# Kernel optimization log

Hardware: AMD Instinct MI355X
Metric: run time of the kernel (lower is better)

## Reference

```python
import jax, jax.numpy as jnp
import numpy as np
import math

EPS = 1e-8
DIM, HEADS, K = 256, 8, 16
HD = DIM // HEADS
B, N, PDIM = 4, 4096, 3


def _layernorm(x, w, b, eps=1e-5):
    m = jnp.mean(x, axis=-1, keepdims=True)
    v = jnp.mean((x - m) ** 2, axis=-1, keepdims=True)
    return (x - m) * jax.lax.rsqrt(v + eps) * w + b


def setup_inputs() -> dict:
    key = jax.random.key(0)
    ks = jax.random.split(key, 16)
    s = 0.02
    d = {
        'x': jax.random.normal(ks[0], (B, N, DIM), jnp.float32),
        'positions': jax.random.uniform(ks[1], (B, N, PDIM), jnp.float32) * 0.5,  # inside unit ball
        'c': jnp.ones((1,), jnp.float32),
        'time_emb': jax.random.normal(ks[2], (B, DIM), jnp.float32),
        'Wq': jax.random.normal(ks[3], (DIM, DIM), jnp.float32) * s,
        'bq': jnp.zeros((DIM,), jnp.float32),
        'Wk': jax.random.normal(ks[4], (DIM, DIM), jnp.float32) * s,
        'bk': jnp.zeros((DIM,), jnp.float32),
        'Wv': jax.random.normal(ks[5], (DIM, DIM), jnp.float32) * s,
        'bv': jnp.zeros((DIM,), jnp.float32),
        'Wo': jax.random.normal(ks[6], (DIM, DIM), jnp.float32) * s,
        'bo': jnp.zeros((DIM,), jnp.float32),
        'W1': jax.random.normal(ks[7], (DIM, 4 * DIM), jnp.float32) * s,
        'b1': jnp.zeros((4 * DIM,), jnp.float32),
        'W2': jax.random.normal(ks[8], (4 * DIM, DIM), jnp.float32) * s,
        'b2': jnp.zeros((DIM,), jnp.float32),
        'ln1_w': jnp.ones((DIM,), jnp.float32),
        'ln1_b': jnp.zeros((DIM,), jnp.float32),
        'ln2_w': jnp.ones((DIM,), jnp.float32),
        'ln2_b': jnp.zeros((DIM,), jnp.float32),
        'log_tau': jnp.zeros((), jnp.float32),
    }
    return d


def _poincare_dist_matrix(pos, c):
    # pos: [B,N,P], c: scalar > 0. Returns [B,N,N] with d[b,i,j] = dist(pos[b,j], pos[b,i])
    sq = jnp.sum(pos ** 2, axis=-1)                      # [B,N]
    diff2 = (sq[:, :, None] + sq[:, None, :]
             - 2.0 * jnp.einsum('bip,bjp->bij', pos, pos))
    diff2 = jnp.maximum(diff2, 0.0)
    num = 2.0 * c * diff2
    den = (1.0 - c * sq[:, :, None]) * (1.0 - c * sq[:, None, :])
    arg = jnp.maximum(1.0 + num / (den + EPS), 1.0)
    return jnp.arccosh(arg) / jnp.sqrt(c)


def reference(x, positions, c, time_emb, Wq, bq, Wk, bk, Wv, bv, Wo, bo,
              W1, b1, W2, b2, ln1_w, ln1_b, ln2_w, ln2_b, log_tau):
    c_s = jnp.squeeze(c)
    x_res = x
    h = _layernorm(x, ln1_w, ln1_b) + time_emb[:, None, :]

    q = (h @ Wq + bq).reshape(B, N, HEADS, HD).transpose(0, 2, 1, 3)  # [B,H,N,hd]
    k = (h @ Wk + bk).reshape(B, N, HEADS, HD).transpose(0, 2, 1, 3)
    v = (h @ Wv + bv).reshape(B, N, HEADS, HD).transpose(0, 2, 1, 3)

    # pairwise hyperbolic distances + kNN (no_grad in original)
    dist = jax.lax.stop_gradient(_poincare_dist_matrix(positions, c_s))  # [B,N,N]
    neg_vals, idx = jax.lax.top_k(-dist, K)          # smallest-K distances
    attn_dists = -neg_vals                            # [B,N,K]

    # gather neighbor keys/values: out[b,h,n,j,d] = k[b,h,idx[b,n,j],d]
    idx_flat = idx.reshape(B, 1, N * K, 1)            # broadcast over heads, hd
    k_g = jnp.take_along_axis(k, idx_flat, axis=2).reshape(B, HEADS, N, K, HD)
    v_g = jnp.take_along_axis(v, idx_flat, axis=2).reshape(B, HEADS, N, K, HD)

    feat = jnp.einsum('bhnd,bhnkd->bhnk', q, k_g) / math.sqrt(HD)
    tau = jnp.exp(log_tau) + EPS
    scores = feat - attn_dists[:, None, :, :] / tau
    probs = jax.nn.softmax(scores, axis=-1)
    attn = jnp.einsum('bhnk,bhnkd->bhnd', probs, v_g)
    attn = attn.transpose(0, 2, 1, 3).reshape(B, N, DIM)

    x2 = x_res + attn @ Wo + bo
    ff = jax.nn.gelu(_layernorm(x2, ln2_w, ln2_b) @ W1 + b1, approximate=False) @ W2 + b2
    return x2 + ff
```

## Files before the change

### kernel.cpp

```cpp
#include <hip/hip_runtime.h>
#include <math.h>

namespace {

constexpr int kBatch = 4;
constexpr int kN = 4096;
constexpr int kDim = 256;
constexpr int kHeads = 8;
constexpr int kK = 16;
constexpr float kEps = 1e-8f;

using u16 = unsigned short;
typedef __attribute__((ext_vector_type(8))) short short8;
typedef __attribute__((ext_vector_type(8))) u16 u16x8;
typedef __attribute__((ext_vector_type(4))) float f32x4;

__device__ __forceinline__ float b2f(u16 u) {
  union { unsigned int i; float f; } x; x.i = ((unsigned int)u) << 16; return x.f;
}
__device__ __forceinline__ u16 f2b(float f) {
  union { float f; unsigned int i; } x; x.f = f;
  unsigned int r = x.i + 0x7fffu + ((x.i >> 16) & 1u);
  return (u16)(r >> 16);
}
__device__ __forceinline__ float gelu_exact(float x) {
  return 0.5f * x * (1.0f + erff(x * 0.70710678118654752f));
}
__device__ __forceinline__ void load_lds16(const u16* g, u16* l) {
  __builtin_amdgcn_global_load_lds(
      (const __attribute__((address_space(1))) unsigned int*)g,
      (__attribute__((address_space(3))) unsigned int*)l, 16, 0, 0);
}

template<bool ADD_TEMB>
__device__ __forceinline__ void ln_body(
    const float* __restrict__ x, const float* __restrict__ w,
    const float* __restrict__ bb, const float* __restrict__ temb,
    u16* __restrict__ out, int gt) {
  int row = gt >> 6;
  int lane = gt & 63;
  const float4* xr = (const float4*)(x + (size_t)row * kDim);
  float4 v = xr[lane];
  float s = v.x + v.y + v.z + v.w;
  #pragma unroll
  for (int off = 32; off; off >>= 1) s += __shfl_xor(s, off);
  float mean = s * (1.0f / kDim);
  float dx = v.x - mean, dy = v.y - mean, dz = v.z - mean, dw = v.w - mean;
  float ss = dx * dx + dy * dy + dz * dz + dw * dw;
  #pragma unroll
  for (int off = 32; off; off >>= 1) ss += __shfl_xor(ss, off);
  float rstd = rsqrtf(ss * (1.0f / kDim) + 1e-5f);
  float4 wv = ((const float4*)w)[lane];
  float4 bv = ((const float4*)bb)[lane];
  float ox = dx * rstd * wv.x + bv.x;
  float oy = dy * rstd * wv.y + bv.y;
  float oz = dz * rstd * wv.z + bv.z;
  float ow = dw * rstd * wv.w + bv.w;
  if (ADD_TEMB) {
    int bi = row >> 12;
    float4 t = ((const float4*)(temb + (size_t)bi * kDim))[lane];
    ox += t.x; oy += t.y; oz += t.z; ow += t.w;
  }
  ushort4 ob;
  ob.x = f2b(ox); ob.y = f2b(oy); ob.z = f2b(oz); ob.w = f2b(ow);
  ((ushort4*)(out + (size_t)row * kDim))[lane] = ob;
}

__global__ __launch_bounds__(1024, 2) void front_kernel(
    const float* __restrict__ pos, const float* __restrict__ cptr,
    int* __restrict__ idx_out, float* __restrict__ dist_out,
    const float* __restrict__ x, const float* __restrict__ ln1w,
    const float* __restrict__ ln1b, const float* __restrict__ temb,
    u16* __restrict__ h_out,
    const float* __restrict__ Wq, const float* __restrict__ Wk,
    const float* __restrict__ Wv, const float* __restrict__ Wo,
    const float* __restrict__ W1, const float* __restrict__ W2,
    u16* __restrict__ Tq, u16* __restrict__ Tk,
    u16* __restrict__ Tv, u16* __restrict__ To,
    u16* __restrict__ T1, u16* __restrict__ T2) {
  __shared__ float4 ps[kN];
  int tid = threadIdx.x;
  int bx = blockIdx.x;

  if (bx >= 1024) {
    if (bx < 1216) {
      int sub = tid >> 8, stid = tid & 255;
      int task = (bx - 1024) * 4 + sub;
      float* tt = (float*)ps + sub * 1056;
      int seg = task >> 8, e = task & 255;
      const float* W; u16* T; int Kin, Nin, kt, nt;
      if (seg == 0) {
        int which = e >> 6, tl = e & 63;
        W = which == 0 ? Wq : which == 1 ? Wk : which == 2 ? Wv : Wo;
        T = which == 0 ? Tq : which == 1 ? Tk : which == 2 ? Tv : To;
        Kin = 256; Nin = 256; kt = tl >> 3; nt = tl & 7;
      } else if (seg == 1) {
        W = W1; T = T1; Kin = 256; Nin = 1024; kt = e >> 5; nt = e & 31;
      } else {
        W = W2; T = T2; Kin = 1024; Nin = 256; kt = e >> 3; nt = e & 7;
      }
      int tx = stid & 31, ty = stid >> 5;
      #pragma unroll
      for (int rr = 0; rr < 4; ++rr) {
        int r = rr * 8 + ty;
        tt[r * 33 + tx] = W[(size_t)(kt * 32 + r) * Nin + nt * 32 + tx];
      }
      __syncthreads();
      #pragma unroll
      for (int rr = 0; rr < 4; ++rr) {
        int r = rr * 8 + ty;
        T[(size_t)(nt * 32 + r) * Kin + kt * 32 + tx] = f2b(tt[tx * 33 + r]);
      }
    } else {
      ln_body<true>(x, ln1w, ln1b, temb, h_out, (bx - 1216) * 1024 + tid);
    }
    return;
  }

  int wave = tid >> 6, ln = tid & 63;
  int row = bx * 16 + wave;
  int b = row >> 12;
  float c = cptr[0];
  const float* pb = pos + (size_t)b * kN * 3;
  for (int j = tid; j < kN; j += 1024) {
    float px = pb[j * 3 + 0], py = pb[j * 3 + 1], pz = pb[j * 3 + 2];
    ps[j] = make_float4(px, py, pz, c * (px * px + py * py + pz * pz));
  }
  __syncthreads();

  int i = row & (kN - 1);
  float4 pi = ps[i];
  float wi = pi.w, oi = 1.0f - wi;
  float sx = 2.0f * c * pi.x, sy = 2.0f * c * pi.y, sz = 2.0f * c * pi.z;

  auto numden = [&](int j, float& num, float& den) {
    float4 pj = ps[j];
    float tt = wi + pj.w;
    tt = fmaf(-sx, pj.x, tt);
    tt = fmaf(-sy, pj.y, tt);
    tt = fmaf(-sz, pj.z, tt);
    num = fmaxf(tt, 0.0f);
    den = fmaf(-oi, pj.w, oi);
  };
  auto packkey = [&](float num, float den, int j) -> unsigned {
    float r = num * __builtin_amdgcn_rcpf(den);
    union { float f; unsigned u; } cv; cv.f = r;
    return (cv.u & 0xFFFFF000u) | (unsigned)j;
  };
  auto inflate = [&](unsigned T) -> float {
    union { unsigned u; float f; } tv; tv.u = T & 0xFFFFF000u;
    return fmaf(tv.f, 0.001f, tv.f);
  };

  float n0, d0;
  numden(ln, n0, d0);
  unsigned lpk = packkey(n0, d0, ln);
  #pragma unroll
  for (int kk = 2; kk <= 64; kk <<= 1) {
    #pragma unroll
    for (int jj = kk >> 1; jj >= 1; jj >>= 1) {
      unsigned ov = (unsigned)__shfl_xor((int)lpk, jj);
      bool keepMin = (((ln & kk) == 0) == ((ln & jj) == 0));
      bool less = ov < lpk;
      if (keepMin ? less : !less) lpk = ov;
    }
  }
  float Tf = inflate((unsigned)__builtin_amdgcn_readlane((int)lpk, 15));

  auto processGroup = [&](float num, float den, int base) {
    unsigned long long m = __ballot(num < Tf * den);
    if (m) {
      unsigned cpk = packkey(num, den, base + ln);
      do {
        int src = __ffsll(m) - 1;
        m &= m - 1;
        unsigned npk = (unsigned)__builtin_amdgcn_readlane((int)cpk, src);
        unsigned pv = (unsigned)__builtin_amdgcn_update_dpp(
            0, (int)lpk, 0x111 , 0xF, 0xF, false);
        bool gt = lpk > npk;
        bool take = gt && ((ln == 0) || (pv <= npk));
        lpk = take ? npk : (gt ? pv : lpk);
      } while (m);
      Tf = inflate((unsigned)__builtin_amdgcn_readlane((int)lpk, 15));
    }
  };

  int t = 1;
  for (; t + 3 < 64; t += 4) {
    float a0, b0, a1, b1, a2, b2, a3, b3;
    numden(ln + (t + 0) * 64, a0, b0);
    numden(ln + (t + 1) * 64, a1, b1);
    numden(ln + (t + 2) * 64, a2, b2);
    numden(ln + (t + 3) * 64, a3, b3);
    processGroup(a0, b0, (t + 0) * 64);
    processGroup(a1, b1, (t + 1) * 64);
    processGroup(a2, b2, (t + 2) * 64);
    processGroup(a3, b3, (t + 3) * 64);
  }
  for (; t < 64; ++t) {
    float a0, b0;
    numden(ln + t * 64, a0, b0);
    processGroup(a0, b0, t * 64);
  }

  if (ln < kK) {
    int j = (int)(lpk & 0xFFFu);
    float4 pj = ps[j];
    float tt = wi + pj.w;
    tt = fmaf(-sx, pj.x, tt);
    tt = fmaf(-sy, pj.y, tt);
    tt = fmaf(-sz, pj.z, tt);
    float num = 2.0f * fmaxf(tt, 0.0f);
    float den = fmaf(-oi, pj.w, oi) + kEps;
    float arg = fmaxf(1.0f + num / den, 1.0f);
    float rs = 1.0f / sqrtf(c);
    idx_out[(size_t)row * kK + ln] = j;
    dist_out[(size_t)row * kK + ln] = acoshf(arg) * rs;
  }
}

template<int EPI, int BN>
__device__ __forceinline__ void gemm_body(
    const u16* __restrict__ A, const u16* __restrict__ Bt,
    const float* __restrict__ bias, const float* __restrict__ R,
    float* __restrict__ Cf, u16* __restrict__ Cbf,
    int N, int K, int bx, int by) {
  constexpr int NI = BN / 32;
  constexpr int BK = 64;
  __shared__ u16 Al[128 * BK];
  __shared__ u16 Bl[BN * BK];
  int tid = threadIdx.x;
  int wv = tid >> 6, ln = tid & 63;
  int wr = wv >> 1, wc = wv & 1;
  int lhi = ln >> 4, llo = ln & 15;
  int bm = bx * 128, bn = by * BN;

  f32x4 zero = {0.f, 0.f, 0.f, 0.f};
  f32x4 acc[4][NI];
  #pragma unroll
  for (int mi = 0; mi < 4; ++mi)
    #pragma unroll
    for (int ni = 0; ni < NI; ++ni) acc[mi][ni] = zero;

  for (int k0 = 0; k0 < K; k0 += BK) {
    if (k0) __syncthreads();
    #pragma unroll
    for (int i = 0; i < 128 * BK / (8 * 256); ++i) {
      int f = i * 256 + tid;
      int r = f >> 3, o = f & 7;
      load_lds16(A + (size_t)(bm + r) * K + k0 + ((o ^ (r & 7)) << 3),
                 &Al[(i * 256 + wv * 64) * 8]);
    }
    #pragma unroll
    for (int i = 0; i < BN * BK / (8 * 256); ++i) {
      int f = i * 256 + tid;
      int r = f >> 3, o = f & 7;
      load_lds16(Bt + (size_t)(bn + r) * K + k0 + ((o ^ (r & 7)) << 3),
                 &Bl[(i * 256 + wv * 64) * 8]);
    }
    __syncthreads();
    #pragma unroll
    for (int ks = 0; ks < BK; ks += 32) {
      short8 af[4], bf[NI];
      #pragma unroll
      for (int mi = 0; mi < 4; ++mi) {
        int row = wr * 64 + mi * 16 + llo;
        int oct = ((ks >> 3) + lhi) ^ (llo & 7);
        af[mi] = *(const short8*)&Al[row * BK + oct * 8];
      }
      #pragma unroll
      for (int ni = 0; ni < NI; ++ni) {
        int row = wc * (BN / 2) + ni * 16 + llo;
        int oct = ((ks >> 3) + lhi) ^ (llo & 7);
        bf[ni] = *(const short8*)&Bl[row * BK + oct * 8];
      }
      #pragma unroll
      for (int mi = 0; mi < 4; ++mi)
        #pragma unroll
        for (int ni = 0; ni < NI; ++ni)
          acc[mi][ni] = __builtin_amdgcn_mfma_f32_16x16x32_bf16(
              af[mi], bf[ni], acc[mi][ni], 0, 0, 0);
    }
  }

  #pragma unroll
  for (int mi = 0; mi < 4; ++mi) {
    #pragma unroll
    for (int r = 0; r < 4; ++r) {
      int row = bm + wr * 64 + mi * 16 + lhi * 4 + r;
      #pragma unroll
      for (int ni = 0; ni < NI; ++ni) {
        int col = bn + wc * (BN / 2) + ni * 16 + llo;
        float val = acc[mi][ni][r] + bias[col];
        if (EPI == 1) {
          val += R[(size_t)row * N + col];
          Cf[(size_t)row * N + col] = val;
        } else {
          if (EPI == 2) val = gelu_exact(val);
          Cbf[(size_t)row * N + col] = f2b(val);
        }
      }
    }
  }
}

template<int EPI, int BN, int NY>
__global__ __launch_bounds__(256) void gemm_swz_kernel(
    const u16* __restrict__ A, const u16* __restrict__ Bt,
    const float* __restrict__ bias, const float* __restrict__ R,
    float* __restrict__ Cf, u16* __restrict__ Cbf, int N, int K) {
  int cpx = gridDim.x >> 3;
  int orig = blockIdx.x;
  int swz = (orig & 7) * cpx + (orig >> 3);
  int bx = swz / NY, by = swz % NY;
  gemm_body<EPI, BN>(A, Bt, bias, R, Cf, Cbf, N, K, bx, by);
}

__global__ __launch_bounds__(256) void qkv_kernel(
    const u16* __restrict__ A,
    const u16* __restrict__ Bq, const u16* __restrict__ Bk, const u16* __restrict__ Bv,
    const float* __restrict__ bq, const float* __restrict__ bk, const float* __restrict__ bv,
    u16* __restrict__ q, u16* __restrict__ k, u16* __restrict__ v) {
  int cpx = gridDim.x >> 3;
  int orig = blockIdx.x;
  int swz = (orig & 7) * cpx + (orig >> 3);
  int bx = swz / 6, y = swz % 6;
  int sel = y >> 1;
  const u16* Bt = sel == 0 ? Bq : sel == 1 ? Bk : Bv;
  const float* bias = sel == 0 ? bq : sel == 1 ? bk : bv;
  u16* C = sel == 0 ? q : sel == 1 ? k : v;
  gemm_body<0, 128>(A, Bt, bias, nullptr, nullptr, C, 256, 256, bx, y & 1);
}

__global__ __launch_bounds__(512) void wo_ln_kernel(
    const u16* __restrict__ A, const u16* __restrict__ Bt,
    const float* __restrict__ bo, const float* __restrict__ xres,
    const float* __restrict__ ln2w, const float* __restrict__ ln2b,
    float* __restrict__ x2, u16* __restrict__ tln) {
  __shared__ u16 Al[64 * 64];
  __shared__ u16 Bl[256 * 64];
  __shared__ float red[4][64][2];
  int tid = threadIdx.x;
  int wv = tid >> 6, ln = tid & 63;
  int wr = wv >> 2, wc = wv & 3;
  int lhi = ln >> 4, llo = ln & 15;
  int bm = blockIdx.x * 64;

  f32x4 zero = {0.f, 0.f, 0.f, 0.f};
  f32x4 acc[2][4];
  #pragma unroll
  for (int mi = 0; mi < 2; ++mi)
    #pragma unroll
    for (int ni = 0; ni < 4; ++ni) acc[mi][ni] = zero;

  for (int k0 = 0; k0 < 256; k0 += 64) {
    if (k0) __syncthreads();
    {
      int f = tid, r = f >> 3, o = f & 7;
      load_lds16(A + (size_t)(bm + r) * 256 + k0 + ((o ^ (r & 7)) << 3),
                 &Al[(wv * 64) * 8]);
    }
    #pragma unroll
    for (int i = 0; i < 4; ++i) {
      int f = i * 512 + tid, r = f >> 3, o = f & 7;
      load_lds16(Bt + (size_t)r * 256 + k0 + ((o ^ (r & 7)) << 3),
                 &Bl[((i * 8 + wv) * 64) * 8]);
    }
    __syncthreads();
    #pragma unroll
    for (int ks = 0; ks < 64; ks += 32) {
      short8 af[2], bf[4];
      #pragma unroll
      for (int mi = 0; mi < 2; ++mi) {
        int row = wr * 32 + mi * 16 + llo;
        int oct = ((ks >> 3) + lhi) ^ (llo & 7);
        af[mi] = *(const short8*)&Al[row * 64 + oct * 8];
      }
      #pragma unroll
      for (int ni = 0; ni < 4; ++ni) {
        int brow = wc * 64 + ni * 16 + llo;
        int oct = ((ks >> 3) + lhi) ^ (llo & 7);
        bf[ni] = *(const short8*)&Bl[brow * 64 + oct * 8];
      }
      #pragma unroll
      for (int mi = 0; mi < 2; ++mi)
        #pragma unroll
        for (int ni = 0; ni < 4; ++ni)
          acc[mi][ni] = __builtin_amdgcn_mfma_f32_16x16x32_bf16(
              af[mi], bf[ni], acc[mi][ni], 0, 0, 0);
    }
  }

  float psum[2][4], psq[2][4];
  #pragma unroll
  for (int mi = 0; mi < 2; ++mi) {
    #pragma unroll
    for (int r = 0; r < 4; ++r) {
      int row = bm + wr * 32 + mi * 16 + lhi * 4 + r;
      float s = 0.0f, q = 0.0f;
      #pragma unroll
      for (int ni = 0; ni < 4; ++ni) {
        int col = wc * 64 + ni * 16 + llo;
        float v = acc[mi][ni][r] + bo[col] + xres[(size_t)row * 256 + col];
        acc[mi][ni][r] = v;
        s += v;
        q = fmaf(v, v, q);
      }
      #pragma unroll
      for (int off = 1; off < 16; off <<= 1) {
        s += __shfl_xor(s, off);
        q += __shfl_xor(q, off);
      }
      psum[mi][r] = s; psq[mi][r] = q;
    }
  }
  if (llo == 0) {
    #pragma unroll
    for (int mi = 0; mi < 2; ++mi)
      #pragma unroll
      for (int r = 0; r < 4; ++r) {
        int rl = wr * 32 + mi * 16 + lhi * 4 + r;
        red[wc][rl][0] = psum[mi][r];
        red[wc][rl][1] = psq[mi][r];
      }
  }
  __syncthreads();
  constexpr float rn = 1.0f / 256.0f;
  #pragma unroll
  for (int mi = 0; mi < 2; ++mi) {
    #pragma unroll
    for (int r = 0; r < 4; ++r) {
      int rl = wr * 32 + mi * 16 + lhi * 4 + r;
      int row = bm + rl;
      float S = red[0][rl][0] + red[1][rl][0] + red[2][rl][0] + red[3][rl][0];
      float Q = red[0][rl][1] + red[1][rl][1] + red[2][rl][1] + red[3][rl][1];
      float mean = S * rn;
      float var = Q * rn - mean * mean;
      float rstd = rsqrtf(var + 1e-5f);
      #pragma unroll
      for (int ni = 0; ni < 4; ++ni) {
        int col = wc * 64 + ni * 16 + llo;
        float v = acc[mi][ni][r];
        x2[(size_t)row * 256 + col] = v;
        tln[(size_t)row * 256 + col] =
            f2b((v - mean) * rstd * ln2w[col] + ln2b[col]);
      }
    }
  }
}

__global__ __launch_bounds__(256) void attn_kernel(
    const u16* __restrict__ q, const u16* __restrict__ k,
    const u16* __restrict__ v, const int* __restrict__ nidx,
    const float* __restrict__ ndist, const float* __restrict__ log_tau,
    u16* __restrict__ out) {
  int t = blockIdx.x * 256 + threadIdx.x;
  int h = t & (kHeads - 1);
  int row = t >> 3;
  int b = row >> 12;
  float rtau = 1.0f / (expf(log_tau[0]) + kEps);
  const u16x8* qr = (const u16x8*)(q + (size_t)row * kDim + h * 32);
  float qf[32];
  #pragma unroll
  for (int cch = 0; cch < 4; ++cch) {
    u16x8 u = qr[cch];
    #pragma unroll
    for (int e = 0; e < 8; ++e) qf[cch * 8 + e] = b2f(u[e]);
  }

  int njs[kK];
  float sc[kK];
  const int* ir = nidx + (size_t)row * kK;
  const float* dr = ndist + (size_t)row * kK;
  float smax = -1e30f;
  #pragma unroll
  for (int j = 0; j < kK; ++j) {
    int nj = ir[j];
    njs[j] = nj;
    const u16x8* kr = (const u16x8*)(k + ((size_t)b * kN + nj) * kDim + h * 32);
    float dot = 0.0f;
    #pragma unroll
    for (int cch = 0; cch < 4; ++cch) {
      u16x8 u = kr[cch];
      #pragma unroll
      for (int e = 0; e < 8; ++e) dot = fmaf(qf[cch * 8 + e], b2f(u[e]), dot);
    }
    float s = dot * 0.17677669529663687f - dr[j] * rtau;
    sc[j] = s;
    smax = fmaxf(smax, s);
  }
  float sum = 0.0f;
  #pragma unroll
  for (int j = 0; j < kK; ++j) { sc[j] = expf(sc[j] - smax); sum += sc[j]; }
  float rsum = 1.0f / sum;
  float o[32];
  #pragma unroll
  for (int d = 0; d < 32; ++d) o[d] = 0.0f;
  #pragma unroll
  for (int j = 0; j < kK; ++j) {
    float p = sc[j] * rsum;
    const u16x8* vr = (const u16x8*)(v + ((size_t)b * kN + njs[j]) * kDim + h * 32);
    #pragma unroll
    for (int cch = 0; cch < 4; ++cch) {
      u16x8 u = vr[cch];
      #pragma unroll
      for (int e = 0; e < 8; ++e) o[cch * 8 + e] = fmaf(p, b2f(u[e]), o[cch * 8 + e]);
    }
  }
  u16x8* orow = (u16x8*)(out + (size_t)row * kDim + h * 32);
  #pragma unroll
  for (int cch = 0; cch < 4; ++cch) {
    u16x8 po;
    #pragma unroll
    for (int e = 0; e < 8; ++e) po[e] = f2b(o[cch * 8 + e]);
    orow[cch] = po;
  }
}

}

extern "C" void kernel_launch(void* const* d_in, const int* in_sizes, int n_in,
                              void* d_out, int out_size, void* d_ws, size_t ws_size,
                              hipStream_t stream) {
  const float* x    = (const float*)d_in[0];
  const float* pos  = (const float*)d_in[1];
  const float* c    = (const float*)d_in[2];
  const float* temb = (const float*)d_in[3];
  const float* Wq   = (const float*)d_in[4];
  const float* bq   = (const float*)d_in[5];
  const float* Wk   = (const float*)d_in[6];
  const float* bk   = (const float*)d_in[7];
  const float* Wv   = (const float*)d_in[8];
  const float* bv   = (const float*)d_in[9];
  const float* Wo   = (const float*)d_in[10];
  const float* bo   = (const float*)d_in[11];
  const float* W1   = (const float*)d_in[12];
  const float* b1   = (const float*)d_in[13];
  const float* W2   = (const float*)d_in[14];
  const float* b2   = (const float*)d_in[15];
  const float* ln1w = (const float*)d_in[16];
  const float* ln1b = (const float*)d_in[17];
  const float* ln2w = (const float*)d_in[18];
  const float* ln2b = (const float*)d_in[19];
  const float* ltau = (const float*)d_in[20];

  const size_t MB = 1ull << 20;
  char* w = (char*)d_ws;
  u16*   h_bf  = (u16*)(w + 0 * MB);
  u16*   qb    = (u16*)(w + 8 * MB);
  u16*   kb    = (u16*)(w + 16 * MB);
  u16*   vb    = (u16*)(w + 24 * MB);
  u16*   attnb = (u16*)(w + 32 * MB);
  float* x2    = (float*)(w + 40 * MB);
  u16*   g_bf  = (u16*)(w + 56 * MB);
  u16*   wq_t  = (u16*)(w + 88 * MB);
  u16*   wk_t  = wq_t + 65536;
  u16*   wv_t  = wq_t + 2 * 65536;
  u16*   wo_t  = wq_t + 3 * 65536;
  u16*   w1_t  = (u16*)(w + 89 * MB);
  u16*   w2_t  = (u16*)(w + 89 * MB + 512 * 1024);
  int*   kidx  = (int*)(w + 90 * MB);
  float* kdst  = (float*)(w + 91 * MB);
  u16*   tln   = h_bf;

  hipLaunchKernelGGL(front_kernel, dim3(2240), dim3(1024), 0, stream,
                     pos, c, kidx, kdst,
                     x, ln1w, ln1b, temb, h_bf,
                     Wq, Wk, Wv, Wo, W1, W2, wq_t, wk_t, wv_t, wo_t, w1_t, w2_t);
  hipLaunchKernelGGL(qkv_kernel, dim3(768), dim3(256), 0, stream,
                     h_bf, wq_t, wk_t, wv_t, bq, bk, bv, qb, kb, vb);
  hipLaunchKernelGGL(attn_kernel, dim3(512), dim3(256), 0, stream,
                     qb, kb, vb, kidx, kdst, ltau, attnb);
  hipLaunchKernelGGL(wo_ln_kernel, dim3(256), dim3(512), 0, stream,
                     attnb, wo_t, bo, x, ln2w, ln2b, x2, tln);
  hipLaunchKernelGGL((gemm_swz_kernel<2, 128, 8>), dim3(1024), dim3(256), 0, stream,
                     tln, w1_t, b1, nullptr, (float*)nullptr, g_bf, 1024, 256);
  hipLaunchKernelGGL((gemm_swz_kernel<1, 64, 4>), dim3(512), dim3(256), 0, stream,
                     g_bf, w2_t, b2, x2, (float*)d_out, (u16*)nullptr, 256, 1024);
}
```

Measured before the change: 163.2 us.

## Fuse kNN attention into Wo projection + LayerNorm kernel via LDS tile

The separate attention kernel is folded into the Wo GEMM + LayerNorm kernel. Each 512-thread block first computes attention for its 64 rows × 8 heads and writes the bf16 result straight into a swizzled 64x256 LDS A-tile, then runs the Wo GEMM from LDS. This removes one launch and the global write/read round trip of the attention output. In exchange, LDS per block grows and the attention phase now runs with only 256 blocks of 512 threads, which lowers parallelism for the gather-heavy part and may reduce occupancy.

New measurement: 161.6 us. No clear change (-1.0%).

```diff
diff --git a/kernel.cpp b/kernel.cpp
--- a/kernel.cpp
+++ b/kernel.cpp
@@ -332,19 +332,86 @@
   gemm_body<0, 128>(A, Bt, bias, nullptr, nullptr, C, 256, 256, bx, y & 1);
 }
 
-__global__ __launch_bounds__(512) void wo_ln_kernel(
-    const u16* __restrict__ A, const u16* __restrict__ Bt,
-    const float* __restrict__ bo, const float* __restrict__ xres,
+__global__ __launch_bounds__(512) void awo_ln_kernel(
+    const u16* __restrict__ q, const u16* __restrict__ k,
+    const u16* __restrict__ v, const int* __restrict__ nidx,
+    const float* __restrict__ ndist, const float* __restrict__ log_tau,
+    const u16* __restrict__ Bt, const float* __restrict__ bo,
+    const float* __restrict__ xres,
     const float* __restrict__ ln2w, const float* __restrict__ ln2b,
     float* __restrict__ x2, u16* __restrict__ tln) {
-  __shared__ u16 Al[64 * 64];
+  __shared__ u16 Al[64 * 256];
   __shared__ u16 Bl[256 * 64];
   __shared__ float red[4][64][2];
   int tid = threadIdx.x;
+  int bm = blockIdx.x * 64;
+
+  {
+    int rl = tid >> 3, h = tid & 7;
+    int row = bm + rl;
+    int b = row >> 12;
+    float rtau = 1.0f / (expf(log_tau[0]) + kEps);
+    const u16x8* qr = (const u16x8*)(q + (size_t)row * kDim + h * 32);
+    float qf[32];
+    #pragma unroll
+    for (int cch = 0; cch < 4; ++cch) {
+      u16x8 u = qr[cch];
+      #pragma unroll
+      for (int e = 0; e < 8; ++e) qf[cch * 8 + e] = b2f(u[e]);
+    }
+    int njs[kK];
+    float sc[kK];
+    const int* ir = nidx + (size_t)row * kK;
+    const float* dr = ndist + (size_t)row * kK;
+    float smax = -1e30f;
+    #pragma unroll
+    for (int j = 0; j < kK; ++j) {
+      int nj = ir[j];
+      njs[j] = nj;
+      const u16x8* kr = (const u16x8*)(k + ((size_t)b * kN + nj) * kDim + h * 32);
+      float dot = 0.0f;
+      #pragma unroll
+      for (int cch = 0; cch < 4; ++cch) {
+        u16x8 u = kr[cch];
+        #pragma unroll
+        for (int e = 0; e < 8; ++e) dot = fmaf(qf[cch * 8 + e], b2f(u[e]), dot);
+      }
+      float s = dot * 0.17677669529663687f - dr[j] * rtau;
+      sc[j] = s;
+      smax = fmaxf(smax, s);
+    }
+    float sum = 0.0f;
+    #pragma unroll
+    for (int j = 0; j < kK; ++j) { sc[j] = expf(sc[j] - smax); sum += sc[j]; }
+    float rsum = 1.0f / sum;
+    float o[32];
+    #pragma unroll
+    for (int d = 0; d < 32; ++d) o[d] = 0.0f;
+    #pragma unroll
+    for (int j = 0; j < kK; ++j) {
+      float p = sc[j] * rsum;
+      const u16x8* vr = (const u16x8*)(v + ((size_t)b * kN + njs[j]) * kDim + h * 32);
+      #pragma unroll
+      for (int cch = 0; cch < 4; ++cch) {
+        u16x8 u = vr[cch];
+        #pragma unroll
+        for (int e = 0; e < 8; ++e) o[cch * 8 + e] = fmaf(p, b2f(u[e]), o[cch * 8 + e]);
+      }
+    }
+    #pragma unroll
+    for (int cch = 0; cch < 4; ++cch) {
+      u16x8 po;
+      #pragma unroll
+      for (int e = 0; e < 8; ++e) po[e] = f2b(o[cch * 8 + e]);
+      int oct = h * 4 + cch;
+      *(u16x8*)&Al[rl * 256 + ((oct ^ (rl & 7)) << 3)] = po;
+    }
+  }
+  __syncthreads();
+
   int wv = tid >> 6, ln = tid & 63;
   int wr = wv >> 2, wc = wv & 3;
   int lhi = ln >> 4, llo = ln & 15;
-  int bm = blockIdx.x * 64;
 
   f32x4 zero = {0.f, 0.f, 0.f, 0.f};
   f32x4 acc[2][4];
@@ -355,11 +422,6 @@
 
   for (int k0 = 0; k0 < 256; k0 += 64) {
     if (k0) __syncthreads();
-    {
-      int f = tid, r = f >> 3, o = f & 7;
-      load_lds16(A + (size_t)(bm + r) * 256 + k0 + ((o ^ (r & 7)) << 3),
-                 &Al[(wv * 64) * 8]);
-    }
     #pragma unroll
     for (int i = 0; i < 4; ++i) {
       int f = i * 512 + tid, r = f >> 3, o = f & 7;
@@ -373,8 +435,8 @@
       #pragma unroll
       for (int mi = 0; mi < 2; ++mi) {
         int row = wr * 32 + mi * 16 + llo;
-        int oct = ((ks >> 3) + lhi) ^ (llo & 7);
-        af[mi] = *(const short8*)&Al[row * 64 + oct * 8];
+        int octg = ((k0 + ks) >> 3) + lhi;
+        af[mi] = *(const short8*)&Al[row * 256 + ((octg ^ (llo & 7)) << 3)];
       }
       #pragma unroll
       for (int ni = 0; ni < 4; ++ni) {
@@ -397,21 +459,21 @@
     #pragma unroll
     for (int r = 0; r < 4; ++r) {
       int row = bm + wr * 32 + mi * 16 + lhi * 4 + r;
-      float s = 0.0f, q = 0.0f;
+      float s = 0.0f, qv = 0.0f;
       #pragma unroll
       for (int ni = 0; ni < 4; ++ni) {
         int col = wc * 64 + ni * 16 + llo;
-        float v = acc[mi][ni][r] + bo[col] + xres[(size_t)row * 256 + col];
-        acc[mi][ni][r] = v;
-        s += v;
-        q = fmaf(v, v, q);
+        float vv = acc[mi][ni][r] + bo[col] + xres[(size_t)row * 256 + col];
+        acc[mi][ni][r] = vv;
+        s += vv;
+        qv = fmaf(vv, vv, qv);
       }
       #pragma unroll
       for (int off = 1; off < 16; off <<= 1) {
         s += __shfl_xor(s, off);
-        q += __shfl_xor(q, off);
-      }
-      psum[mi][r] = s; psq[mi][r] = q;
+        qv += __shfl_xor(qv, off);
+      }
+      psum[mi][r] = s; psq[mi][r] = qv;
     }
   }
   if (llo == 0) {
@@ -440,80 +502,12 @@
       #pragma unroll
       for (int ni = 0; ni < 4; ++ni) {
         int col = wc * 64 + ni * 16 + llo;
-        float v = acc[mi][ni][r];
-        x2[(size_t)row * 256 + col] = v;
+        float vv = acc[mi][ni][r];
+        x2[(size_t)row * 256 + col] = vv;
         tln[(size_t)row * 256 + col] =
-            f2b((v - mean) * rstd * ln2w[col] + ln2b[col]);
-      }
-    }
-  }
-}
-
-__global__ __launch_bounds__(256) void attn_kernel(
-    const u16* __restrict__ q, const u16* __restrict__ k,
-    const u16* __restrict__ v, const int* __restrict__ nidx,
-    const float* __restrict__ ndist, const float* __restrict__ log_tau,
-    u16* __restrict__ out) {
-  int t = blockIdx.x * 256 + threadIdx.x;
-  int h = t & (kHeads - 1);
-  int row = t >> 3;
-  int b = row >> 12;
-  float rtau = 1.0f / (expf(log_tau[0]) + kEps);
-  const u16x8* qr = (const u16x8*)(q + (size_t)row * kDim + h * 32);
-  float qf[32];
-  #pragma unroll
-  for (int cch = 0; cch < 4; ++cch) {
-    u16x8 u = qr[cch];
-    #pragma unroll
-    for (int e = 0; e < 8; ++e) qf[cch * 8 + e] = b2f(u[e]);
-  }
-
-  int njs[kK];
-  float sc[kK];
-  const int* ir = nidx + (size_t)row * kK;
-  const float* dr = ndist + (size_t)row * kK;
-  float smax = -1e30f;
-  #pragma unroll
-  for (int j = 0; j < kK; ++j) {
-    int nj = ir[j];
-    njs[j] = nj;
-    const u16x8* kr = (const u16x8*)(k + ((size_t)b * kN + nj) * kDim + h * 32);
-    float dot = 0.0f;
-    #pragma unroll
-    for (int cch = 0; cch < 4; ++cch) {
-      u16x8 u = kr[cch];
-      #pragma unroll
-      for (int e = 0; e < 8; ++e) dot = fmaf(qf[cch * 8 + e], b2f(u[e]), dot);
-    }
-    float s = dot * 0.17677669529663687f - dr[j] * rtau;
-    sc[j] = s;
-    smax = fmaxf(smax, s);
-  }
-  float sum = 0.0f;
-  #pragma unroll
-  for (int j = 0; j < kK; ++j) { sc[j] = expf(sc[j] - smax); sum += sc[j]; }
-  float rsum = 1.0f / sum;
-  float o[32];
-  #pragma unroll
-  for (int d = 0; d < 32; ++d) o[d] = 0.0f;
-  #pragma unroll
-  for (int j = 0; j < kK; ++j) {
-    float p = sc[j] * rsum;
-    const u16x8* vr = (const u16x8*)(v + ((size_t)b * kN + njs[j]) * kDim + h * 32);
-    #pragma unroll
-    for (int cch = 0; cch < 4; ++cch) {
-      u16x8 u = vr[cch];
-      #pragma unroll
-      for (int e = 0; e < 8; ++e) o[cch * 8 + e] = fmaf(p, b2f(u[e]), o[cch * 8 + e]);
-    }
-  }
-  u16x8* orow = (u16x8*)(out + (size_t)row * kDim + h * 32);
-  #pragma unroll
-  for (int cch = 0; cch < 4; ++cch) {
-    u16x8 po;
-    #pragma unroll
-    for (int e = 0; e < 8; ++e) po[e] = f2b(o[cch * 8 + e]);
-    orow[cch] = po;
+            f2b((vv - mean) * rstd * ln2w[col] + ln2b[col]);
+      }
+    }
   }
 }
 
@@ -550,7 +544,6 @@
   u16*   qb    = (u16*)(w + 8 * MB);
   u16*   kb    = (u16*)(w + 16 * MB);
   u16*   vb    = (u16*)(w + 24 * MB);
-  u16*   attnb = (u16*)(w + 32 * MB);
   float* x2    = (float*)(w + 40 * MB);
   u16*   g_bf  = (u16*)(w + 56 * MB);
   u16*   wq_t  = (u16*)(w + 88 * MB);
@@ -569,10 +562,9 @@
                      Wq, Wk, Wv, Wo, W1, W2, wq_t, wk_t, wv_t, wo_t, w1_t, w2_t);
   hipLaunchKernelGGL(qkv_kernel, dim3(768), dim3(256), 0, stream,
                      h_bf, wq_t, wk_t, wv_t, bq, bk, bv, qb, kb, vb);
-  hipLaunchKernelGGL(attn_kernel, dim3(512), dim3(256), 0, stream,
-                     qb, kb, vb, kidx, kdst, ltau, attnb);
-  hipLaunchKernelGGL(wo_ln_kernel, dim3(256), dim3(512), 0, stream,
-                     attnb, wo_t, bo, x, ln2w, ln2b, x2, tln);
+  hipLaunchKernelGGL(awo_ln_kernel, dim3(256), dim3(512), 0, stream,
+                     qb, kb, vb, kidx, kdst, ltau,
+                     wo_t, bo, x, ln2w, ln2b, x2, tln);
   hipLaunchKernelGGL((gemm_swz_kernel<2, 128, 8>), dim3(1024), dim3(256), 0, stream,
                      tln, w1_t, b1, nullptr, (float*)nullptr, g_bf, 1024, 256);
   hipLaunchKernelGGL((gemm_swz_kernel<1, 64, 4>), dim3(512), dim3(256), 0, stream,
```
